# Optimization experiments

Hardware: AMD Instinct MI355X
Metric: run time of the kernel (lower is better)

## Reference

```python
import jax, jax.numpy as jnp
import numpy as np

B, T, D, H, FF = 4, 2048, 1024, 16, 4096
HD = D // H
EPS = 1e-5


def setup_inputs() -> dict:
    key = jax.random.key(0)
    ks = jax.random.split(key, 10)
    s = lambda k, shape, fan: jax.random.normal(k, shape, jnp.float32) * (1.0 / np.sqrt(fan))
    return {
        "x": jax.random.normal(ks[0], (B, T, D), jnp.float32),
        "ln1_g": jnp.ones((D,), jnp.float32),
        "ln1_b": jnp.zeros((D,), jnp.float32),
        "qkv_w": s(ks[1], (D, 3 * D), D),
        "qkv_b": jnp.zeros((3 * D,), jnp.float32),
        "proj_w": s(ks[2], (D, D), D),
        "proj_b": jnp.zeros((D,), jnp.float32),
        "ln2_g": jnp.ones((D,), jnp.float32),
        "ln2_b": jnp.zeros((D,), jnp.float32),
        "ff1_w": s(ks[3], (D, FF), D),
        "ff1_b": jnp.zeros((FF,), jnp.float32),
        "ff2_w": s(ks[4], (FF, D), FF),
        "ff2_b": jnp.zeros((D,), jnp.float32),
    }


def _layernorm(x, g, b):
    mu = jnp.mean(x, axis=-1, keepdims=True)
    var = jnp.mean(jnp.square(x - mu), axis=-1, keepdims=True)
    return (x - mu) * jax.lax.rsqrt(var + EPS) * g + b


def reference(x, ln1_g, ln1_b, qkv_w, qkv_b, proj_w, proj_b,
              ln2_g, ln2_b, ff1_w, ff1_b, ff2_w, ff2_b):
    # --- attention sublayer ---
    h = _layernorm(x, ln1_g, ln1_b)
    qkv = h @ qkv_w + qkv_b                      # [B,T,3D]
    q, k, v = jnp.split(qkv, 3, axis=-1)
    q = q.reshape(B, T, H, HD).transpose(0, 2, 1, 3)  # [B,H,T,hd]
    k = k.reshape(B, T, H, HD).transpose(0, 2, 1, 3)
    v = v.reshape(B, T, H, HD).transpose(0, 2, 1, 3)
    att = jnp.einsum('bhqd,bhkd->bhqk', q, k) / np.sqrt(HD)
    causal = jnp.tril(jnp.ones((T, T), bool))
    att = jnp.where(causal, att, jnp.finfo(att.dtype).min)
    att = jax.nn.softmax(att, axis=-1)
    out = jnp.einsum('bhqk,bhkd->bhqd', att, v)  # [B,H,T,hd]
    out = out.transpose(0, 2, 1, 3).reshape(B, T, D)
    x = x + out @ proj_w + proj_b
    # --- MLP sublayer ---
    h = _layernorm(x, ln2_g, ln2_b)
    h = jax.nn.gelu(h @ ff1_w + ff1_b, approximate=True)
    x = x + h @ ff2_w + ff2_b
    return x
```

## Files before the change

### kernel.cpp

```cpp
#include <hip/hip_runtime.h>

typedef __attribute__((ext_vector_type(4))) float f32x4;
typedef __attribute__((ext_vector_type(8))) short s16x8;
typedef __attribute__((ext_vector_type(4))) unsigned short u16x4;

#define DEV __device__ __forceinline__

DEV unsigned short f2bf(float f) {
  unsigned int u = __float_as_uint(f);
  return (unsigned short)((u + 0x7FFFu + ((u >> 16) & 1u)) >> 16);
}

DEV void gload_lds16(const void* g, void* l) {
  __builtin_amdgcn_global_load_lds(
      (const __attribute__((address_space(1))) unsigned int*)g,
      (__attribute__((address_space(3))) unsigned int*)l, 16, 0, 0);
}

__global__ __launch_bounds__(256) void ln_kernel(
    const float* __restrict__ x, const float* __restrict__ gam,
    const float* __restrict__ bet, unsigned short* __restrict__ o)
{
  const int row = blockIdx.x;
  const int tid = threadIdx.x;
  f32x4 v = *(const f32x4*)(x + (size_t)row * 1024 + tid * 4);
  float s = v[0] + v[1] + v[2] + v[3];
  float s2 = v[0]*v[0] + v[1]*v[1] + v[2]*v[2] + v[3]*v[3];
  #pragma unroll
  for (int m = 1; m < 64; m <<= 1) { s += __shfl_xor(s, m); s2 += __shfl_xor(s2, m); }
  __shared__ float ps[4], ps2[4];
  const int wid = tid >> 6, lane = tid & 63;
  if (lane == 0) { ps[wid] = s; ps2[wid] = s2; }
  __syncthreads();
  s = ps[0] + ps[1] + ps[2] + ps[3];
  s2 = ps2[0] + ps2[1] + ps2[2] + ps2[3];
  const float mu = s * (1.0f / 1024.0f);
  const float rstd = rsqrtf(s2 * (1.0f / 1024.0f) - mu * mu + 1e-5f);
  f32x4 g4 = *(const f32x4*)(gam + tid * 4);
  f32x4 b4 = *(const f32x4*)(bet + tid * 4);
  u16x4 ov;
  #pragma unroll
  for (int j = 0; j < 4; j++) ov[j] = f2bf((v[j] - mu) * rstd * g4[j] + b4[j]);
  *(u16x4*)(o + (size_t)row * 1024 + tid * 4) = ov;
}

__global__ __launch_bounds__(256) void transpose_kernel(
    const float* __restrict__ W, unsigned short* __restrict__ WT, int K, int N)
{
  __shared__ float tile[64][65];
  const int n0 = blockIdx.x * 64, k0 = blockIdx.y * 64;
  const int c = threadIdx.x & 63, r0 = threadIdx.x >> 6;
  #pragma unroll
  for (int r = r0; r < 64; r += 4)
    tile[r][c] = W[(size_t)(k0 + r) * N + n0 + c];
  __syncthreads();
  #pragma unroll
  for (int r = r0; r < 64; r += 4)
    WT[(size_t)(n0 + r) * K + k0 + c] = f2bf(tile[c][r]);
}

template <int MODE>
__global__ __launch_bounds__(512) void gemm8_kernel(
    const unsigned short* __restrict__ A, const unsigned short* __restrict__ WT,
    const float* __restrict__ bias, const float* resid, void* outp,
    int M, int N, int K)
{
  __shared__ unsigned short lds[3 * 24576];
  const int tid = threadIdx.x;
  const int lane = tid & 63, wid = tid >> 6;
  const int l15 = lane & 15, l4 = lane >> 4;
  const int wm = wid >> 2, wn = wid & 3;
  const int tiles_n = N >> 8;
  const int cpx = gridDim.x >> 3;
  const int id = (blockIdx.x & 7) * cpx + (blockIdx.x >> 3);
  const int bm = id / tiles_n, bn = id % tiles_n;
  const int NT = K >> 6;

  const int srow = tid >> 3;
  const int scol = ((tid & 7) ^ (srow & 7)) * 8;
  const unsigned short* Asrc = A  + (size_t)(bm * 128 + srow) * K + scol;
  const unsigned short* Bsrc = WT + (size_t)(bn * 256 + srow) * K + scol;
  const size_t j64 = (size_t)64 * K;
  const int dwave = wid * 1024;

#define STAGE(t_, ss_) do { \
    char* base_ = (char*)lds + (ss_) * 49152 + dwave; \
    const unsigned short* sA_ = Asrc + (size_t)(t_) * 64; \
    const unsigned short* sB_ = Bsrc + (size_t)(t_) * 64; \
    gload_lds16(sA_,            base_); \
    gload_lds16(sA_ + j64,      base_ + 8192); \
    gload_lds16(sB_,            base_ + 16384); \
    gload_lds16(sB_ + j64,      base_ + 16384 + 8192); \
    gload_lds16(sB_ + 2 * j64,  base_ + 16384 + 16384); \
    gload_lds16(sB_ + 3 * j64,  base_ + 16384 + 24576); \
  } while (0)

  f32x4 acc[4][4] = {};

  const int arow0 = wm * 64 + l15;
  const int brow0 = wn * 64 + l15;
  const int cswz = l15 & 7;

  STAGE(0, 0);
  STAGE(1, 1);
  asm volatile("s_waitcnt vmcnt(6)" ::: "memory");
  __builtin_amdgcn_s_barrier();

  int cs = 0, ss = 2;
  for (int t = 0; t < NT; ++t) {
    const unsigned short* sa = lds + cs * 24576;
    const unsigned short* sb = sa + 8192;
    s16x8 bf[4][2];
    #pragma unroll
    for (int p = 0; p < 2; ++p) {
      s16x8 af[2][2];
      #pragma unroll
      for (int mi = 0; mi < 2; ++mi)
        #pragma unroll
        for (int ks = 0; ks < 2; ++ks) {
          const int row = arow0 + (p * 2 + mi) * 16;
          af[mi][ks] = *(const s16x8*)&sa[row * 64 + (((ks * 4 + l4) ^ cswz) * 8)];
        }
      if (p == 0) {
        #pragma unroll
        for (int nf = 0; nf < 4; ++nf)
          #pragma unroll
          for (int ks = 0; ks < 2; ++ks) {
            const int row = brow0 + nf * 16;
            bf[nf][ks] = *(const s16x8*)&sb[row * 64 + (((ks * 4 + l4) ^ cswz) * 8)];
          }
        if (t + 2 < NT) STAGE(t + 2, ss);
      }
      __builtin_amdgcn_s_barrier();
      asm volatile("s_waitcnt lgkmcnt(0)" ::: "memory");
      __builtin_amdgcn_sched_barrier(0);
      __builtin_amdgcn_s_setprio(1);
      #pragma unroll
      for (int mi = 0; mi < 2; ++mi)
        #pragma unroll
        for (int nf = 0; nf < 4; ++nf)
          #pragma unroll
          for (int ks = 0; ks < 2; ++ks)
            acc[p * 2 + mi][nf] = __builtin_amdgcn_mfma_f32_16x16x32_bf16(
                af[mi][ks], bf[nf][ks], acc[p * 2 + mi][nf], 0, 0, 0);
      __builtin_amdgcn_s_setprio(0);
      if (p == 1) {
        if (t + 2 < NT)      { asm volatile("s_waitcnt vmcnt(6)" ::: "memory"); }
        else if (t + 1 < NT) { asm volatile("s_waitcnt vmcnt(0)" ::: "memory"); }
      }
      __builtin_amdgcn_s_barrier();
    }
    cs = (cs == 2) ? 0 : cs + 1;
    ss = (ss == 2) ? 0 : ss + 1;
  }
#undef STAGE

  #pragma unroll
  for (int nf = 0; nf < 4; nf++) {
    const int col = bn * 256 + wn * 64 + nf * 16 + l15;
    const float bv = bias[col];
    #pragma unroll
    for (int mf = 0; mf < 4; mf++) {
      #pragma unroll
      for (int r = 0; r < 4; r++) {
        const int row = bm * 128 + wm * 64 + mf * 16 + l4 * 4 + r;
        const size_t off = (size_t)row * N + col;
        float v = acc[mf][nf][r] + bv;
        if (MODE == 1) {
          ((float*)outp)[off] = v + resid[off];
        } else if (MODE == 2) {
          const float tt = __expf(1.5957691216f * (v + 0.044715f * v * v * v));
          ((unsigned short*)outp)[off] = f2bf(v - v / (tt + 1.0f));
        } else {
          ((unsigned short*)outp)[off] = f2bf(v);
        }
      }
    }
  }
}

struct AttnState {
  f32x4 o[4];
  float m, l;
};

DEV void attn_tile(const s16x8* qf, const unsigned short* Ks,
                   const unsigned short* Vt, unsigned short* Pw,
                   AttnState& st, int kv0, int qg, int l15, int l4, bool need_mask)
{
  f32x4 sa[4];
  #pragma unroll
  for (int cb = 0; cb < 4; cb++) sa[cb] = (f32x4){0.f, 0.f, 0.f, 0.f};
  __builtin_amdgcn_s_setprio(1);
  #pragma unroll
  for (int ks = 0; ks < 2; ++ks) {
    #pragma unroll
    for (int cb = 0; cb < 4; cb++) {
      const int kvr = cb * 16 + l15;
      s16x8 bk = *(const s16x8*)&Ks[kvr * 64 + ((ks * 32 + l4 * 8) ^ ((kvr & 7) << 3))];
      sa[cb] = __builtin_amdgcn_mfma_f32_16x16x32_bf16(bk, qf[ks], sa[cb], 0, 0, 0);
    }
  }
  __builtin_amdgcn_s_setprio(0);
  float mx = -3.0e38f;
  const int thr = qg - kv0 - l4 * 4;
  #pragma unroll
  for (int cb = 0; cb < 4; cb++)
    #pragma unroll
    for (int r = 0; r < 4; r++) {
      float sv = sa[cb][r] * 0.125f;
      if (need_mask && (cb * 16 + r > thr)) sv = -3.0e38f;
      sa[cb][r] = sv;
      mx = fmaxf(mx, sv);
    }
  mx = fmaxf(mx, __shfl_xor(mx, 16));
  mx = fmaxf(mx, __shfl_xor(mx, 32));
  const float mnew = fmaxf(st.m, mx);
  const float alpha = __expf(st.m - mnew);
  st.m = mnew;
  float rsum = 0.f;
  #pragma unroll
  for (int cb = 0; cb < 4; cb++) {
    u16x4 pw;
    #pragma unroll
    for (int r = 0; r < 4; r++) {
      const float p = __expf(sa[cb][r] - mnew);
      rsum += p;
      pw[r] = f2bf(p);
    }
    *(u16x4*)&Pw[l15 * 64 + ((cb * 16 + l4 * 4) ^ ((l15 & 7) << 3))] = pw;
  }
  rsum += __shfl_xor(rsum, 16);
  rsum += __shfl_xor(rsum, 32);
  st.l = st.l * alpha + rsum;
  #pragma unroll
  for (int r = 0; r < 4; r++) {
    const float ar = __shfl(alpha, l4 * 4 + r);
    #pragma unroll
    for (int cb = 0; cb < 4; cb++) st.o[cb][r] *= ar;
  }
  asm volatile("s_waitcnt lgkmcnt(0)" ::: "memory");
  __builtin_amdgcn_s_setprio(1);
  #pragma unroll
  for (int ks = 0; ks < 2; ++ks) {
    s16x8 pa = *(const s16x8*)&Pw[l15 * 64 + ((ks * 32 + l4 * 8) ^ ((l15 & 7) << 3))];
    #pragma unroll
    for (int cb = 0; cb < 4; cb++) {
      const int d = cb * 16 + l15;
      s16x8 vf = *(const s16x8*)&Vt[d * 64 + ((ks * 32 + l4 * 8) ^ (((d >> 2) & 7) << 3))];
      st.o[cb] = __builtin_amdgcn_mfma_f32_16x16x32_bf16(pa, vf, st.o[cb], 0, 0, 0);
    }
  }
  __builtin_amdgcn_s_setprio(0);
}

DEV void attn_write(unsigned short* orow, const AttnState& st, int l15, int l4) {
  const float invl = 1.0f / st.l;
  #pragma unroll
  for (int r = 0; r < 4; r++) {
    const float ir = __shfl(invl, l4 * 4 + r);
    #pragma unroll
    for (int cb = 0; cb < 4; cb++)
      orow[(l4 * 4 + r) * 1024 + cb * 16 + l15] = f2bf(st.o[cb][r] * ir);
  }
}

__global__ __launch_bounds__(256) void attn_kernel(
    const unsigned short* __restrict__ qkv, unsigned short* __restrict__ outb)
{
  __shared__ unsigned short Ks[64 * 64];
  __shared__ unsigned short Vt[64 * 64];
  __shared__ unsigned short Ps[2][4][16 * 64];
  const int pid = blockIdx.x;
  const int qA = pid, qB = 31 - pid;
  const int bh = blockIdx.y;
  const int b = bh >> 4, h = bh & 15;
  const int tid = threadIdx.x, lane = tid & 63, wid = tid >> 6;
  const int l15 = lane & 15, l4 = lane >> 4;
  const size_t base = (size_t)b * 2048 * 3072 + (size_t)h * 64;
  const unsigned short* Qb = qkv + base;
  const unsigned short* Kb = qkv + base + 1024;
  const unsigned short* Vb = qkv + base + 2048;

  s16x8 qfA[2], qfB[2];
  {
    const unsigned short* qr = Qb + (size_t)(qA * 64 + wid * 16 + l15) * 3072 + l4 * 8;
    qfA[0] = *(const s16x8*)qr;
    qfA[1] = *(const s16x8*)(qr + 32);
    qr = Qb + (size_t)(qB * 64 + wid * 16 + l15) * 3072 + l4 * 8;
    qfB[0] = *(const s16x8*)qr;
    qfB[1] = *(const s16x8*)(qr + 32);
  }
  AttnState sA, sB;
  #pragma unroll
  for (int cb = 0; cb < 4; cb++) {
    sA.o[cb] = (f32x4){0.f, 0.f, 0.f, 0.f};
    sB.o[cb] = (f32x4){0.f, 0.f, 0.f, 0.f};
  }
  sA.m = -1e30f; sA.l = 0.f; sB.m = -1e30f; sB.l = 0.f;
  const int qgA = qA * 64 + wid * 16 + l15;
  const int qgB = qB * 64 + wid * 16 + l15;

  for (int kvb = 0; kvb <= qB; ++kvb) {
    const int kv0 = kvb * 64;
    __syncthreads();
    #pragma unroll
    for (int s = 0; s < 2; ++s) {
      const int c = s * 256 + tid;
      const int kv = c >> 3;
      const int dsrc = ((c & 7) * 8) ^ ((kv & 7) << 3);
      gload_lds16(Kb + (size_t)(kv0 + kv) * 3072 + dsrc,
                  Ks + (size_t)(c & ~63) * 8);
    }
    #pragma unroll
    for (int it = 0; it < 4; ++it) {
      const int cc = tid + 256 * it;
      const int vkv = cc >> 4;
      const int vd = (cc & 15) * 4;
      u16x4 vv = *(const u16x4*)(Vb + (size_t)(kv0 + vkv) * 3072 + vd);
      #pragma unroll
      for (int j = 0; j < 4; j++) {
        const int d = vd + j;
        Vt[d * 64 + (vkv ^ (((d >> 2) & 7) << 3))] = vv[j];
      }
    }
    __syncthreads();

    if (kvb <= qA)
      attn_tile(qfA, Ks, Vt, Ps[0][wid], sA, kv0, qgA, l15, l4,
                kv0 + 63 > qA * 64 + wid * 16);
    attn_tile(qfB, Ks, Vt, Ps[1][wid], sB, kv0, qgB, l15, l4,
              kv0 + 63 > qB * 64 + wid * 16);
  }
  attn_write(outb + ((size_t)b * 2048 + qA * 64 + wid * 16) * 1024 + h * 64, sA, l15, l4);
  attn_write(outb + ((size_t)b * 2048 + qB * 64 + wid * 16) * 1024 + h * 64, sB, l15, l4);
}

extern "C" void kernel_launch(void* const* d_in, const int* in_sizes, int n_in,
                              void* d_out, int out_size, void* d_ws, size_t ws_size,
                              hipStream_t stream) {
  const float* x      = (const float*)d_in[0];
  const float* ln1_g  = (const float*)d_in[1];
  const float* ln1_b  = (const float*)d_in[2];
  const float* qkv_w  = (const float*)d_in[3];
  const float* qkv_b  = (const float*)d_in[4];
  const float* proj_w = (const float*)d_in[5];
  const float* proj_b = (const float*)d_in[6];
  const float* ln2_g  = (const float*)d_in[7];
  const float* ln2_b  = (const float*)d_in[8];
  const float* ff1_w  = (const float*)d_in[9];
  const float* ff1_b  = (const float*)d_in[10];
  const float* ff2_w  = (const float*)d_in[11];
  const float* ff2_b  = (const float*)d_in[12];
  float* out = (float*)d_out;

  char* ws = (char*)d_ws;
  size_t off = 0;
  unsigned short* wbuf   = (unsigned short*)(ws + off); off += (size_t)4096 * 1024 * 2;
  unsigned short* hbuf   = (unsigned short*)(ws + off); off += (size_t)8192 * 1024 * 2;
  unsigned short* qkvbuf = (unsigned short*)(ws + off); off += (size_t)8192 * 3072 * 2;
  unsigned short* gbuf   = (unsigned short*)(ws + off);

  ln_kernel<<<8192, 256, 0, stream>>>(x, ln1_g, ln1_b, hbuf);
  transpose_kernel<<<dim3(3072 / 64, 1024 / 64), 256, 0, stream>>>(qkv_w, wbuf, 1024, 3072);
  gemm8_kernel<0><<<dim3(64 * 12), 512, 0, stream>>>(hbuf, wbuf, qkv_b, nullptr, qkvbuf,
                                                     8192, 3072, 1024);
  attn_kernel<<<dim3(16, 64), 256, 0, stream>>>(qkvbuf, hbuf);
  transpose_kernel<<<dim3(1024 / 64, 1024 / 64), 256, 0, stream>>>(proj_w, wbuf, 1024, 1024);
  gemm8_kernel<1><<<dim3(64 * 4), 512, 0, stream>>>(hbuf, wbuf, proj_b, x, out,
                                                    8192, 1024, 1024);
  ln_kernel<<<8192, 256, 0, stream>>>(out, ln2_g, ln2_b, hbuf);
  transpose_kernel<<<dim3(4096 / 64, 1024 / 64), 256, 0, stream>>>(ff1_w, wbuf, 1024, 4096);
  gemm8_kernel<2><<<dim3(64 * 16), 512, 0, stream>>>(hbuf, wbuf, ff1_b, nullptr, gbuf,
                                                     8192, 4096, 1024);
  transpose_kernel<<<dim3(1024 / 64, 4096 / 64), 256, 0, stream>>>(ff2_w, wbuf, 4096, 1024);
  gemm8_kernel<1><<<dim3(64 * 4), 512, 0, stream>>>(gbuf, wbuf, ff2_b, out, out,
                                                    8192, 1024, 4096);
}
```

Before: 471.2 us.

## Double-buffer K/V prefetch in attention, lazy softmax rescale, exp2 intrinsics

The attention loop now double-buffers K in LDS and holds the next V tile in registers, so global loads for tile k+1 overlap compute on tile k. Explicit barriers and waitcnts replace the __syncthreads pairs. The softmax works in base 2 with a pre-scaled log2e factor and uses raw v_exp/v_rcp. It skips the running-max update and the accumulator rescale while the new max stays within a threshold of the old one. GELU is rewritten as v*sigmoid using exp2 and rcp. This cuts the exponential and rescale work on the attention critical path, but the manual vmcnt counting and lazy rescale add correctness and overflow risk.

```diff
diff --git a/kernel.cpp b/kernel.cpp
--- a/kernel.cpp
+++ b/kernel.cpp
@@ -9,6 +9,13 @@
 DEV unsigned short f2bf(float f) {
   unsigned int u = __float_as_uint(f);
   return (unsigned short)((u + 0x7FFFu + ((u >> 16) & 1u)) >> 16);
+}
+
+DEV float exp2_asm(float x) {
+  float r; asm("v_exp_f32 %0, %1" : "=v"(r) : "v"(x)); return r;
+}
+DEV float rcp_asm(float x) {
+  float r; asm("v_rcp_f32 %0, %1" : "=v"(r) : "v"(x)); return r;
 }
 
 DEV void gload_lds16(const void* g, void* l) {
@@ -169,8 +176,9 @@
         if (MODE == 1) {
           ((float*)outp)[off] = v + resid[off];
         } else if (MODE == 2) {
-          const float tt = __expf(1.5957691216f * (v + 0.044715f * v * v * v));
-          ((unsigned short*)outp)[off] = f2bf(v - v / (tt + 1.0f));
+          const float u = v + 0.044715f * v * v * v;
+          const float e = exp2_asm(-2.3022010f * u);
+          ((unsigned short*)outp)[off] = f2bf(v * rcp_asm(1.0f + e));
         } else {
           ((unsigned short*)outp)[off] = f2bf(v);
         }
@@ -208,23 +216,22 @@
   for (int cb = 0; cb < 4; cb++)
     #pragma unroll
     for (int r = 0; r < 4; r++) {
-      float sv = sa[cb][r] * 0.125f;
+      float sv = sa[cb][r] * 0.18033688f;
       if (need_mask && (cb * 16 + r > thr)) sv = -3.0e38f;
       sa[cb][r] = sv;
       mx = fmaxf(mx, sv);
     }
   mx = fmaxf(mx, __shfl_xor(mx, 16));
   mx = fmaxf(mx, __shfl_xor(mx, 32));
-  const float mnew = fmaxf(st.m, mx);
-  const float alpha = __expf(st.m - mnew);
-  st.m = mnew;
+  const bool skip = __all(mx <= st.m + 11.5f);
+  const float mnew = skip ? st.m : fmaxf(st.m, mx);
   float rsum = 0.f;
   #pragma unroll
   for (int cb = 0; cb < 4; cb++) {
     u16x4 pw;
     #pragma unroll
     for (int r = 0; r < 4; r++) {
-      const float p = __expf(sa[cb][r] - mnew);
+      const float p = exp2_asm(sa[cb][r] - mnew);
       rsum += p;
       pw[r] = f2bf(p);
     }
@@ -232,12 +239,18 @@
   }
   rsum += __shfl_xor(rsum, 16);
   rsum += __shfl_xor(rsum, 32);
-  st.l = st.l * alpha + rsum;
-  #pragma unroll
-  for (int r = 0; r < 4; r++) {
-    const float ar = __shfl(alpha, l4 * 4 + r);
-    #pragma unroll
-    for (int cb = 0; cb < 4; cb++) st.o[cb][r] *= ar;
+  if (skip) {
+    st.l += rsum;
+  } else {
+    const float alpha = exp2_asm(st.m - mnew);
+    st.l = st.l * alpha + rsum;
+    st.m = mnew;
+    #pragma unroll
+    for (int r = 0; r < 4; r++) {
+      const float ar = __shfl(alpha, l4 * 4 + r);
+      #pragma unroll
+      for (int cb = 0; cb < 4; cb++) st.o[cb][r] *= ar;
+    }
   }
   asm volatile("s_waitcnt lgkmcnt(0)" ::: "memory");
   __builtin_amdgcn_s_setprio(1);
@@ -255,7 +268,7 @@
 }
 
 DEV void attn_write(unsigned short* orow, const AttnState& st, int l15, int l4) {
-  const float invl = 1.0f / st.l;
+  const float invl = rcp_asm(st.l);
   #pragma unroll
   for (int r = 0; r < 4; r++) {
     const float ir = __shfl(invl, l4 * 4 + r);
@@ -268,7 +281,7 @@
 __global__ __launch_bounds__(256) void attn_kernel(
     const unsigned short* __restrict__ qkv, unsigned short* __restrict__ outb)
 {
-  __shared__ unsigned short Ks[64 * 64];
+  __shared__ unsigned short Ks[2][64 * 64];
   __shared__ unsigned short Vt[64 * 64];
   __shared__ unsigned short Ps[2][4][16 * 64];
   const int pid = blockIdx.x;
@@ -291,6 +304,21 @@
     qfB[0] = *(const s16x8*)qr;
     qfB[1] = *(const s16x8*)(qr + 32);
   }
+
+  u16x4 vv[4];
+  #pragma unroll
+  for (int it = 0; it < 4; ++it) {
+    const int cc = tid + 256 * it;
+    vv[it] = *(const u16x4*)(Vb + (size_t)(cc >> 4) * 3072 + (cc & 15) * 4);
+  }
+  #pragma unroll
+  for (int s = 0; s < 2; ++s) {
+    const int c = s * 256 + tid;
+    const int kv = c >> 3;
+    const int dsrc = ((c & 7) * 8) ^ ((kv & 7) << 3);
+    gload_lds16(Kb + (size_t)kv * 3072 + dsrc, &Ks[0][(size_t)(c & ~63) * 8]);
+  }
+
   AttnState sA, sB;
   #pragma unroll
   for (int cb = 0; cb < 4; cb++) {
@@ -302,34 +330,47 @@
   const int qgB = qB * 64 + wid * 16 + l15;
 
   for (int kvb = 0; kvb <= qB; ++kvb) {
+    const int cur = kvb & 1;
     const int kv0 = kvb * 64;
-    __syncthreads();
-    #pragma unroll
-    for (int s = 0; s < 2; ++s) {
-      const int c = s * 256 + tid;
-      const int kv = c >> 3;
-      const int dsrc = ((c & 7) * 8) ^ ((kv & 7) << 3);
-      gload_lds16(Kb + (size_t)(kv0 + kv) * 3072 + dsrc,
-                  Ks + (size_t)(c & ~63) * 8);
-    }
+    __builtin_amdgcn_s_barrier();
+    asm volatile("s_waitcnt vmcnt(2)" ::: "memory");
     #pragma unroll
     for (int it = 0; it < 4; ++it) {
       const int cc = tid + 256 * it;
       const int vkv = cc >> 4;
       const int vd = (cc & 15) * 4;
-      u16x4 vv = *(const u16x4*)(Vb + (size_t)(kv0 + vkv) * 3072 + vd);
       #pragma unroll
       for (int j = 0; j < 4; j++) {
         const int d = vd + j;
-        Vt[d * 64 + (vkv ^ (((d >> 2) & 7) << 3))] = vv[j];
-      }
-    }
-    __syncthreads();
-
+        Vt[d * 64 + (vkv ^ (((d >> 2) & 7) << 3))] = vv[it][j];
+      }
+    }
+    if (kvb < qB) {
+      #pragma unroll
+      for (int it = 0; it < 4; ++it) {
+        const int cc = tid + 256 * it;
+        vv[it] = *(const u16x4*)(Vb + (size_t)((kvb + 1) * 64 + (cc >> 4)) * 3072 + (cc & 15) * 4);
+      }
+      asm volatile("s_waitcnt vmcnt(4)" ::: "memory");
+    } else {
+      asm volatile("s_waitcnt vmcnt(0)" ::: "memory");
+    }
+    asm volatile("s_waitcnt lgkmcnt(0)" ::: "memory");
+    __builtin_amdgcn_s_barrier();
+    if (kvb < qB) {
+      #pragma unroll
+      for (int s = 0; s < 2; ++s) {
+        const int c = s * 256 + tid;
+        const int kv = c >> 3;
+        const int dsrc = ((c & 7) * 8) ^ ((kv & 7) << 3);
+        gload_lds16(Kb + (size_t)((kvb + 1) * 64 + kv) * 3072 + dsrc,
+                    &Ks[cur ^ 1][(size_t)(c & ~63) * 8]);
+      }
+    }
     if (kvb <= qA)
-      attn_tile(qfA, Ks, Vt, Ps[0][wid], sA, kv0, qgA, l15, l4,
+      attn_tile(qfA, Ks[cur], Vt, Ps[0][wid], sA, kv0, qgA, l15, l4,
                 kv0 + 63 > qA * 64 + wid * 16);
-    attn_tile(qfB, Ks, Vt, Ps[1][wid], sB, kv0, qgB, l15, l4,
+    attn_tile(qfB, Ks[cur], Vt, Ps[1][wid], sB, kv0, qgB, l15, l4,
               kv0 + 63 > qB * 64 + wid * 16);
   }
   attn_write(outb + ((size_t)b * 2048 + qA * 64 + wid * 16) * 1024 + h * 64, sA, l15, l4);
```

New measurement: 459.5 us. -2.5%, faster.
